# Optimization experiments

Measured on AMD Instinct MI355X. Metric: run time of the kernel, lower is better.

The kernel has to match this reference:

```python
import jax, jax.numpy as jnp
import numpy as np

L_KERNELS = 15
STRIDE = 1
DIMS = [60, 72, 86, 86, 71, 59]  # indim=4*15, then *1.2,*1.2, mid, /1.2,/1.2 per __init__


def setup_inputs() -> dict:
    key = jax.random.key(0)
    ks = jax.random.split(key, 13)
    B, C, L, K = 16, 4, 1000, 64
    inp = {"x": jax.random.normal(ks[0], (B, C, L), jnp.float32)}
    for i in range(5):
        di, do = DIMS[i], DIMS[i + 1]
        inp[f"w{i}"] = jax.random.normal(ks[1 + 2 * i], (K, di, do), jnp.float32) * (1.0 / np.sqrt(di))
        inp[f"b{i}"] = jax.random.normal(ks[2 + 2 * i], (K, do), jnp.float32) * 0.01
    inp["head_w"] = jax.random.normal(ks[11], (DIMS[5], 1), jnp.float32) * (1.0 / np.sqrt(DIMS[5]))
    inp["head_b"] = jax.random.normal(ks[12], (1,), jnp.float32) * 0.01
    return inp


def reference(x, w0, b0, w1, b1, w2, b2, w3, b3, w4, b4, head_w, head_b):
    B, C, L = x.shape
    l, s = L_KERNELS, STRIDE
    n_out = (L - l) // s + 1
    # unfold: (B, C, n_out, l) via gather of sliding windows
    idx = jnp.arange(n_out)[:, None] * s + jnp.arange(l)[None, :]
    xw = x[:, :, idx]
    # transpose(-2,-3) then flatten(start_dim=3): (B, n_out, C*l)
    xw = jnp.transpose(xw, (0, 2, 1, 3)).reshape(B, n_out, C * l)
    # per-kernel FC stack: broadcast-mul+sum in torch == grouped matmul here
    h = jax.nn.gelu(jnp.einsum('bld,kde->bkle', xw, w0) + b0[None, :, None, :], approximate=False)
    for w, b in ((w1, b1), (w2, b2), (w3, b3), (w4, b4)):
        h = jax.nn.gelu(jnp.einsum('bkld,kde->bkle', h, w) + b[None, :, None, :], approximate=False)
    out = (h @ head_w + head_b).squeeze(-1)  # (B, K, n_out)
    return out
```

## Files before the change

### kernel.cpp

```cpp
#include <hip/hip_runtime.h>

typedef _Float16 f16;
typedef __attribute__((ext_vector_type(8))) _Float16 f16x8;
typedef __attribute__((ext_vector_type(2))) __fp16 hf16x2;
typedef __attribute__((ext_vector_type(4))) float f32x4;

constexpr int C_ = 4, L_ = 1000, K_ = 64, NOUT = 986, NPOS = 16 * 986;
constexpr int TPB  = 256;
constexpr int MTB  = 128;
constexpr int NBLK = (NPOS + MTB - 1) / MTB;
constexpr int AST  = 104;
constexpr int ACT_EL  = MTB * AST;
constexpr size_t SMEM_BYTES = (size_t)ACT_EL * 2 + 480 * 4 + 64 * 4;

constexpr size_t WOFF[5]  = {0, 638976, 1277952, 1916928, 2555904};
constexpr int    WROWS[5] = {80, 96, 96, 80, 64};
constexpr int    DIv[5]   = {60, 72, 86, 86, 71};
constexpr int    DOv[5]   = {72, 86, 86, 71, 59};
constexpr size_t WTOT    = WOFF[4] + (size_t)K_ * 96 * AST;
constexpr size_t ACT_WS  = WTOT;
constexpr size_t WS_NEED = (WTOT + (size_t)NBLK * ACT_EL) * 2;

constexpr int WUNITS = 5 * K_ * 2;
constexpr int AUNITS = NBLK * 2;

__device__ __forceinline__ float gelu_f(float x) {
    float x2 = x * x;
    float ei = x * __builtin_fmaf(-0.1029433270f, x2, -2.3022082020f);
    float e  = __builtin_amdgcn_exp2f(ei);
    return x * __builtin_amdgcn_rcpf(e + 1.0f);
}

template<int MT>
__device__ __forceinline__ void pre_a(const f16* __restrict__ wsrc, f16x8 (&ap)[6],
                                      int li, int q) {
#pragma unroll
    for (int mt = 0; mt < MT; mt++)
        ap[mt] = *(const f16x8*)(wsrc + (mt * 16 + li) * AST + q * 8);
}

template<int KSTEPS, int MT>
__device__ __forceinline__ void layer_mm_p(const f16* __restrict__ actw,
                                           const f16* __restrict__ wsrc,
                                           const f16x8 (&ap)[6],
                                           f32x4 (&acc)[MT][2],
                                           const float* __restrict__ bl, int li, int q) {
#pragma unroll
    for (int mt = 0; mt < MT; mt++) {
        f32x4 bb = *(const f32x4*)(bl + mt * 16 + q * 4);
#pragma unroll
        for (int nt = 0; nt < 2; nt++) acc[mt][nt] = bb;
    }
#pragma unroll
    for (int ks = 0; ks < KSTEPS; ks++) {
        const int koff = ks * 32 + q * 8;
        f16x8 a[MT], b[2];
#pragma unroll
        for (int mt = 0; mt < MT; mt++)
            a[mt] = (ks == 0) ? ap[mt]
                              : *(const f16x8*)(wsrc + (mt * 16 + li) * AST + koff);
#pragma unroll
        for (int nt = 0; nt < 2; nt++)
            b[nt] = *(const f16x8*)(actw + (nt * 16 + li) * AST + koff);
#pragma unroll
        for (int mt = 0; mt < MT; mt++)
#pragma unroll
            for (int nt = 0; nt < 2; nt++)
                acc[mt][nt] = __builtin_amdgcn_mfma_f32_16x16x32_f16(a[mt], b[nt], acc[mt][nt], 0, 0, 0);
    }
}

template<int MT>
__device__ __forceinline__ void epilogue(f32x4 (&acc)[MT][2], f16* __restrict__ actw,
                                         int li, int q) {
#pragma unroll
    for (int mt = 0; mt < MT; mt++) {
        const int eb = mt * 16 + q * 4;
#pragma unroll
        for (int nt = 0; nt < 2; nt++) {
            union { hf16x2 h[2]; unsigned long long u; } pk;
            pk.h[0] = __builtin_amdgcn_cvt_pkrtz(gelu_f(acc[mt][nt][0]),
                                                 gelu_f(acc[mt][nt][1]));
            pk.h[1] = __builtin_amdgcn_cvt_pkrtz(gelu_f(acc[mt][nt][2]),
                                                 gelu_f(acc[mt][nt][3]));
            f16* dst = actw + (nt * 16 + li) * AST + eb;
            *(unsigned long long*)dst = pk.u;
        }
    }
}

template<int L>
__device__ __forceinline__ void prep_one_half(const float* __restrict__ wsrc0,
                                              f16* __restrict__ ws, f16* __restrict__ wl,
                                              int k, int h, int tid) {
    constexpr int DI = DIv[L], DO = DOv[L], RW = WROWS[L];
    const float* wsrc = wsrc0 + (size_t)k * DI * DO;
    constexpr int TOT = DI * DO;
    constexpr int NIT = (TOT + 255) / 256;
    float v[NIT];
#pragma unroll
    for (int it = 0; it < NIT; it++) {
        int i = tid + it * 256;
        v[it] = (i < TOT) ? wsrc[i] : 0.f;
    }
#pragma unroll
    for (int it = 0; it < NIT; it++) {
        int i = tid + it * 256;
        if (i < TOT) {
            int d = i / DO, e = i - d * DO;
            wl[d * 87 + e] = (f16)v[it];
        }
    }
    __syncthreads();
    f16* dst = ws + WOFF[L] + (size_t)k * 96 * AST;
    constexpr int HCH = (RW / 2) * 13;
    constexpr int NIT2 = (HCH + 255) / 256;
#pragma unroll
    for (int it = 0; it < NIT2; it++) {
        int c0 = tid + it * 256;
        if (c0 < HCH) {
            int c = h * HCH + c0;
            int e = c / 13, db = (c - e * 13) * 8;
            f16x8 vv;
#pragma unroll
            for (int j = 0; j < 8; j++) {
                int d = db + j;
                vv[j] = (e < DO && d < DI) ? wl[d * 87 + e] : (f16)0.f;
            }
            *(f16x8*)(dst + (size_t)c * 8) = vv;
        }
    }
}

__device__ __forceinline__ void prep_act_half(const float* __restrict__ x,
                                              f16* __restrict__ dst0, int m, int h, int tid) {
    if (m >= NBLK) return;
    f16* dst = dst0 + (size_t)m * ACT_EL;
    const int base = m * MTB;
    constexpr int HCHK = MTB * 13 / 2;
    for (int i0 = tid; i0 < HCHK; i0 += 256) {
        int i = h * HCHK + i0;
        int r = i / 13, cc = (i - r * 13) * 8;
        int p = base + r; if (p > NPOS - 1) p = NPOS - 1;
        int b = p / NOUT, pos = p - b * NOUT;
        f16x8 vv;
#pragma unroll
        for (int j = 0; j < 8; j++) {
            int c = cc + j;
            float v = 0.f;
            if (c < 60) { int ch = c / 15, jj = c - ch * 15; v = x[(size_t)(b * C_ + ch) * L_ + pos + jj]; }
            vv[j] = (f16)v;
        }
        *(f16x8*)(dst + (size_t)r * AST + cc) = vv;
    }
}

__global__ __launch_bounds__(256) void prep_all(
    const float* __restrict__ w0, const float* __restrict__ w1, const float* __restrict__ w2,
    const float* __restrict__ w3, const float* __restrict__ w4,
    const float* __restrict__ x, f16* __restrict__ ws) {
    __shared__ f16 wl[86 * 87];
    const int tid = threadIdx.x, u = blockIdx.x;
    if (u < WUNITS) {
        const int k = (u >> 1) & 63, h = u & 1;
        switch (u >> 7) {
            case 0: prep_one_half<0>(w0, ws, wl, k, h, tid); break;
            case 1: prep_one_half<1>(w1, ws, wl, k, h, tid); break;
            case 2: prep_one_half<2>(w2, ws, wl, k, h, tid); break;
            case 3: prep_one_half<3>(w3, ws, wl, k, h, tid); break;
            default: prep_one_half<4>(w4, ws, wl, k, h, tid); break;
        }
    } else {
        const int v = u - WUNITS;
        prep_act_half(x, ws + ACT_WS, v >> 1, v & 1, tid);
    }
}

template<bool PRE>
__global__ __launch_bounds__(TPB, 5) void mlp_main(
    const float* __restrict__ x,
    const float* __restrict__ b0, const float* __restrict__ b1, const float* __restrict__ b2,
    const float* __restrict__ b3, const float* __restrict__ b4,
    const float* __restrict__ hw, const float* __restrict__ hb,
    const f16* __restrict__ ws, float* __restrict__ out) {
    extern __shared__ char smemraw[];
    f16*   act   = (f16*)smemraw;
    float* biasl = (float*)(act + ACT_EL);
    float* headl = biasl + 480;

    const int tid = threadIdx.x, k = blockIdx.x, mblk = blockIdx.y;
    const int wv = tid >> 6, lane = tid & 63, li = lane & 15, q = lane >> 4;
    const int base = mblk * MTB;
    f16* actw = act + (wv * 32) * AST;
    const f16* wk = ws + (size_t)k * 96 * AST;

    f16x8 ap[6];
    pre_a<5>(wk + WOFF[0], ap, li, q);

    for (int i = tid; i < 480; i += TPB) {
        int l = i / 96, e = i - l * 96;
        const float* bg = (l == 0) ? b0 : (l == 1) ? b1 : (l == 2) ? b2 : (l == 3) ? b3 : b4;
        int DO = (l == 0) ? 72 : (l == 1) ? 86 : (l == 2) ? 86 : (l == 3) ? 71 : 59;
        biasl[i] = (e < DO) ? bg[k * DO + e] : 0.f;
    }
    if (tid < 64) headl[tid] = (tid < 59) ? hw[tid] : 0.f;

    if constexpr (PRE) {
        const f16* src = ws + ACT_WS + (size_t)mblk * ACT_EL;
        for (int c = wv; c < 26; c += 4) {
            __builtin_amdgcn_global_load_lds(
                (const __attribute__((address_space(1))) void*)(src + c * 512 + lane * 8),
                (__attribute__((address_space(3))) void*)(act + c * 512), 16, 0, 0);
        }
    } else {
        const int b0i = base / NOUT;
        const int thr = (b0i + 1) * NOUT;
        for (int i = tid; i < 64 * MTB; i += TPB) {
            int d = i >> 7, r = i & (MTB - 1);
            int p = base + r; if (p > NPOS - 1) p = NPOS - 1;
            int b = (p >= thr) ? b0i + 1 : b0i;
            int pos = p - b * NOUT;
            float v = 0.f;
            if (d < 60) { int c = d / 15, j = d - c * 15; v = x[(size_t)(b * C_ + c) * L_ + pos + j]; }
            act[r * AST + d] = (f16)v;
        }
        for (int i = tid; i < MTB * 2; i += TPB) {
            int r = i >> 1, cc = (i & 1) << 3;
            *(f16x8*)(act + r * AST + 80 + cc) = f16x8{0,0,0,0,0,0,0,0};
        }
    }
    const float hb0 = hb[0];
    __syncthreads();

    f32x4 acc[6][2];
    f32x4 (&acc5)[5][2] = reinterpret_cast<f32x4 (&)[5][2]>(acc);

    layer_mm_p<2, 5>(actw, wk + WOFF[0], ap, acc5, biasl + 0 * 96, li, q);
    pre_a<6>(wk + WOFF[1], ap, li, q);
    epilogue<5>(acc5, actw, li, q);
    layer_mm_p<3, 6>(actw, wk + WOFF[1], ap, acc, biasl + 1 * 96, li, q);
    pre_a<6>(wk + WOFF[2], ap, li, q);
    epilogue<6>(acc, actw, li, q);
    layer_mm_p<3, 6>(actw, wk + WOFF[2], ap, acc, biasl + 2 * 96, li, q);
    pre_a<5>(wk + WOFF[3], ap, li, q);
    epilogue<6>(acc, actw, li, q);
    layer_mm_p<3, 5>(actw, wk + WOFF[3], ap, acc5, biasl + 3 * 96, li, q);
    pre_a<4>(wk + WOFF[4], ap, li, q);
    epilogue<5>(acc5, actw, li, q);

    f32x4 acc4[4][2];
    layer_mm_p<3, 4>(actw, wk + WOFF[4], ap, acc4, biasl + 4 * 96, li, q);
    float sum[2] = {0.f, 0.f};
#pragma unroll
    for (int mt = 0; mt < 4; mt++) {
        const int eb = mt * 16 + q * 4;
        f32x4 hh = *(const f32x4*)(headl + eb);
#pragma unroll
        for (int nt = 0; nt < 2; nt++) {
#pragma unroll
            for (int r = 0; r < 4; r++)
                sum[nt] += gelu_f(acc4[mt][nt][r]) * hh[r];
        }
    }
#pragma unroll
    for (int nt = 0; nt < 2; nt++) {
        float s = sum[nt];
        s += __shfl_xor(s, 16);
        s += __shfl_xor(s, 32);
        s += hb0;
        if (lane < 16) {
            int p = base + wv * 32 + nt * 16 + lane;
            if (p < NPOS) {
                int b = p / NOUT, pos = p - b * NOUT;
                out[((size_t)(b * K_ + k)) * NOUT + pos] = s;
            }
        }
    }
}

extern "C" void kernel_launch(void* const* d_in, const int* in_sizes, int n_in,
                              void* d_out, int out_size, void* d_ws, size_t ws_size,
                              hipStream_t stream) {
    const float* x  = (const float*)d_in[0];
    const float* w0 = (const float*)d_in[1];  const float* b0 = (const float*)d_in[2];
    const float* w1 = (const float*)d_in[3];  const float* b1 = (const float*)d_in[4];
    const float* w2 = (const float*)d_in[5];  const float* b2 = (const float*)d_in[6];
    const float* w3 = (const float*)d_in[7];  const float* b3 = (const float*)d_in[8];
    const float* w4 = (const float*)d_in[9];  const float* b4 = (const float*)d_in[10];
    const float* hw = (const float*)d_in[11]; const float* hb = (const float*)d_in[12];
    float* out = (float*)d_out;
    f16* ws = (f16*)d_ws;

    const bool pre = (ws_size >= WS_NEED);

    if (pre) {
        (void)hipFuncSetAttribute((const void*)mlp_main<true>,
                                  hipFuncAttributeMaxDynamicSharedMemorySize, (int)SMEM_BYTES);
        prep_all<<<dim3(WUNITS + AUNITS), 256, 0, stream>>>(w0, w1, w2, w3, w4, x, ws);
        mlp_main<true><<<dim3(K_, NBLK), TPB, SMEM_BYTES, stream>>>(
            x, b0, b1, b2, b3, b4, hw, hb, ws, out);
    } else {
        (void)hipFuncSetAttribute((const void*)mlp_main<false>,
                                  hipFuncAttributeMaxDynamicSharedMemorySize, (int)SMEM_BYTES);
        prep_all<<<dim3(WUNITS), 256, 0, stream>>>(w0, w1, w2, w3, w4, x, ws);
        mlp_main<false><<<dim3(K_, NBLK), TPB, SMEM_BYTES, stream>>>(
            x, b0, b1, b2, b3, b4, hw, hb, ws, out);
    }
}
```

Measured before the change: 253.6 us.

## Halve position tile to 64 rows per block and drop weight-fragment prefetch

Cuts the position tile per block from 128 to 64, so each wave handles 16 positions with one B fragment instead of two. It also drops the cross-layer prefetch of the first weight k-step and raises the launch-bounds occupancy hint from 5 to 8. The smaller tile lowers LDS and register use to fit more resident blocks and doubles the grid, at the cost of half the weight reuse per LDS-loaded A fragment. The loss of the prefetch exposes weight-load latency at the start of each layer.

```diff
diff --git a/kernel.cpp b/kernel.cpp
--- a/kernel.cpp
+++ b/kernel.cpp
@@ -7,7 +7,7 @@
 
 constexpr int C_ = 4, L_ = 1000, K_ = 64, NOUT = 986, NPOS = 16 * 986;
 constexpr int TPB  = 256;
-constexpr int MTB  = 128;
+constexpr int MTB  = 64;
 constexpr int NBLK = (NPOS + MTB - 1) / MTB;
 constexpr int AST  = 104;
 constexpr int ACT_EL  = MTB * AST;
@@ -22,7 +22,7 @@
 constexpr size_t WS_NEED = (WTOT + (size_t)NBLK * ACT_EL) * 2;
 
 constexpr int WUNITS = 5 * K_ * 2;
-constexpr int AUNITS = NBLK * 2;
+constexpr int AUNITS = NBLK;
 
 __device__ __forceinline__ float gelu_f(float x) {
     float x2 = x * x;
@@ -31,61 +31,38 @@
     return x * __builtin_amdgcn_rcpf(e + 1.0f);
 }
 
-template<int MT>
-__device__ __forceinline__ void pre_a(const f16* __restrict__ wsrc, f16x8 (&ap)[6],
-                                      int li, int q) {
+template<int KSTEPS, int MT>
+__device__ __forceinline__ void layer_mm(const f16* __restrict__ actw,
+                                         const f16* __restrict__ wsrc,
+                                         f32x4 (&acc)[MT],
+                                         const float* __restrict__ bl, int li, int q) {
 #pragma unroll
     for (int mt = 0; mt < MT; mt++)
-        ap[mt] = *(const f16x8*)(wsrc + (mt * 16 + li) * AST + q * 8);
-}
-
-template<int KSTEPS, int MT>
-__device__ __forceinline__ void layer_mm_p(const f16* __restrict__ actw,
-                                           const f16* __restrict__ wsrc,
-                                           const f16x8 (&ap)[6],
-                                           f32x4 (&acc)[MT][2],
-                                           const float* __restrict__ bl, int li, int q) {
-#pragma unroll
-    for (int mt = 0; mt < MT; mt++) {
-        f32x4 bb = *(const f32x4*)(bl + mt * 16 + q * 4);
-#pragma unroll
-        for (int nt = 0; nt < 2; nt++) acc[mt][nt] = bb;
-    }
+        acc[mt] = *(const f32x4*)(bl + mt * 16 + q * 4);
 #pragma unroll
     for (int ks = 0; ks < KSTEPS; ks++) {
         const int koff = ks * 32 + q * 8;
-        f16x8 a[MT], b[2];
+        f16x8 a[MT];
 #pragma unroll
         for (int mt = 0; mt < MT; mt++)
-            a[mt] = (ks == 0) ? ap[mt]
-                              : *(const f16x8*)(wsrc + (mt * 16 + li) * AST + koff);
-#pragma unroll
-        for (int nt = 0; nt < 2; nt++)
-            b[nt] = *(const f16x8*)(actw + (nt * 16 + li) * AST + koff);
+            a[mt] = *(const f16x8*)(wsrc + (mt * 16 + li) * AST + koff);
+        f16x8 b = *(const f16x8*)(actw + li * AST + koff);
 #pragma unroll
         for (int mt = 0; mt < MT; mt++)
-#pragma unroll
-            for (int nt = 0; nt < 2; nt++)
-                acc[mt][nt] = __builtin_amdgcn_mfma_f32_16x16x32_f16(a[mt], b[nt], acc[mt][nt], 0, 0, 0);
+            acc[mt] = __builtin_amdgcn_mfma_f32_16x16x32_f16(a[mt], b, acc[mt], 0, 0, 0);
     }
 }
 
 template<int MT>
-__device__ __forceinline__ void epilogue(f32x4 (&acc)[MT][2], f16* __restrict__ actw,
+__device__ __forceinline__ void epilogue(f32x4 (&acc)[MT], f16* __restrict__ actw,
                                          int li, int q) {
 #pragma unroll
     for (int mt = 0; mt < MT; mt++) {
         const int eb = mt * 16 + q * 4;
-#pragma unroll
-        for (int nt = 0; nt < 2; nt++) {
-            union { hf16x2 h[2]; unsigned long long u; } pk;
-            pk.h[0] = __builtin_amdgcn_cvt_pkrtz(gelu_f(acc[mt][nt][0]),
-                                                 gelu_f(acc[mt][nt][1]));
-            pk.h[1] = __builtin_amdgcn_cvt_pkrtz(gelu_f(acc[mt][nt][2]),
-                                                 gelu_f(acc[mt][nt][3]));
-            f16* dst = actw + (nt * 16 + li) * AST + eb;
-            *(unsigned long long*)dst = pk.u;
-        }
+        union { hf16x2 h[2]; unsigned long long u; } pk;
+        pk.h[0] = __builtin_amdgcn_cvt_pkrtz(gelu_f(acc[mt][0]), gelu_f(acc[mt][1]));
+        pk.h[1] = __builtin_amdgcn_cvt_pkrtz(gelu_f(acc[mt][2]), gelu_f(acc[mt][3]));
+        *(unsigned long long*)(actw + li * AST + eb) = pk.u;
     }
 }
 
@@ -132,14 +109,13 @@
     }
 }
 
-__device__ __forceinline__ void prep_act_half(const float* __restrict__ x,
-                                              f16* __restrict__ dst0, int m, int h, int tid) {
+__device__ __forceinline__ void prep_act(const float* __restrict__ x, f16* __restrict__ dst0,
+                                         int m, int tid) {
     if (m >= NBLK) return;
     f16* dst = dst0 + (size_t)m * ACT_EL;
     const int base = m * MTB;
-    constexpr int HCHK = MTB * 13 / 2;
-    for (int i0 = tid; i0 < HCHK; i0 += 256) {
-        int i = h * HCHK + i0;
+    constexpr int CHK = MTB * 13;
+    for (int i = tid; i < CHK; i += 256) {
         int r = i / 13, cc = (i - r * 13) * 8;
         int p = base + r; if (p > NPOS - 1) p = NPOS - 1;
         int b = p / NOUT, pos = p - b * NOUT;
@@ -171,13 +147,12 @@
             default: prep_one_half<4>(w4, ws, wl, k, h, tid); break;
         }
     } else {
-        const int v = u - WUNITS;
-        prep_act_half(x, ws + ACT_WS, v >> 1, v & 1, tid);
+        prep_act(x, ws + ACT_WS, u - WUNITS, tid);
     }
 }
 
 template<bool PRE>
-__global__ __launch_bounds__(TPB, 5) void mlp_main(
+__global__ __launch_bounds__(TPB, 8) void mlp_main(
     const float* __restrict__ x,
     const float* __restrict__ b0, const float* __restrict__ b1, const float* __restrict__ b2,
     const float* __restrict__ b3, const float* __restrict__ b4,
@@ -191,11 +166,8 @@
     const int tid = threadIdx.x, k = blockIdx.x, mblk = blockIdx.y;
     const int wv = tid >> 6, lane = tid & 63, li = lane & 15, q = lane >> 4;
     const int base = mblk * MTB;
-    f16* actw = act + (wv * 32) * AST;
+    f16* actw = act + (wv * 16) * AST;
     const f16* wk = ws + (size_t)k * 96 * AST;
-
-    f16x8 ap[6];
-    pre_a<5>(wk + WOFF[0], ap, li, q);
 
     for (int i = tid; i < 480; i += TPB) {
         int l = i / 96, e = i - l * 96;
@@ -207,7 +179,7 @@
 
     if constexpr (PRE) {
         const f16* src = ws + ACT_WS + (size_t)mblk * ACT_EL;
-        for (int c = wv; c < 26; c += 4) {
+        for (int c = wv; c < 13; c += 4) {
             __builtin_amdgcn_global_load_lds(
                 (const __attribute__((address_space(1))) void*)(src + c * 512 + lane * 8),
                 (__attribute__((address_space(3))) void*)(act + c * 512), 16, 0, 0);
@@ -216,7 +188,7 @@
         const int b0i = base / NOUT;
         const int thr = (b0i + 1) * NOUT;
         for (int i = tid; i < 64 * MTB; i += TPB) {
-            int d = i >> 7, r = i & (MTB - 1);
+            int d = i >> 6, r = i & (MTB - 1);
             int p = base + r; if (p > NPOS - 1) p = NPOS - 1;
             int b = (p >= thr) ? b0i + 1 : b0i;
             int pos = p - b * NOUT;
@@ -232,48 +204,37 @@
     const float hb0 = hb[0];
     __syncthreads();
 
-    f32x4 acc[6][2];
-    f32x4 (&acc5)[5][2] = reinterpret_cast<f32x4 (&)[5][2]>(acc);
-
-    layer_mm_p<2, 5>(actw, wk + WOFF[0], ap, acc5, biasl + 0 * 96, li, q);
-    pre_a<6>(wk + WOFF[1], ap, li, q);
+    f32x4 acc[6];
+    f32x4 (&acc5)[5] = reinterpret_cast<f32x4 (&)[5]>(acc);
+
+    layer_mm<2, 5>(actw, wk + WOFF[0], acc5, biasl + 0 * 96, li, q);
     epilogue<5>(acc5, actw, li, q);
-    layer_mm_p<3, 6>(actw, wk + WOFF[1], ap, acc, biasl + 1 * 96, li, q);
-    pre_a<6>(wk + WOFF[2], ap, li, q);
+    layer_mm<3, 6>(actw, wk + WOFF[1], acc,  biasl + 1 * 96, li, q);
     epilogue<6>(acc, actw, li, q);
-    layer_mm_p<3, 6>(actw, wk + WOFF[2], ap, acc, biasl + 2 * 96, li, q);
-    pre_a<5>(wk + WOFF[3], ap, li, q);
+    layer_mm<3, 6>(actw, wk + WOFF[2], acc,  biasl + 2 * 96, li, q);
     epilogue<6>(acc, actw, li, q);
-    layer_mm_p<3, 5>(actw, wk + WOFF[3], ap, acc5, biasl + 3 * 96, li, q);
-    pre_a<4>(wk + WOFF[4], ap, li, q);
+    layer_mm<3, 5>(actw, wk + WOFF[3], acc5, biasl + 3 * 96, li, q);
     epilogue<5>(acc5, actw, li, q);
 
-    f32x4 acc4[4][2];
-    layer_mm_p<3, 4>(actw, wk + WOFF[4], ap, acc4, biasl + 4 * 96, li, q);
-    float sum[2] = {0.f, 0.f};
+    f32x4 acc4[4];
+    layer_mm<3, 4>(actw, wk + WOFF[4], acc4, biasl + 4 * 96, li, q);
+    float sum = 0.f;
 #pragma unroll
     for (int mt = 0; mt < 4; mt++) {
         const int eb = mt * 16 + q * 4;
         f32x4 hh = *(const f32x4*)(headl + eb);
 #pragma unroll
-        for (int nt = 0; nt < 2; nt++) {
-#pragma unroll
-            for (int r = 0; r < 4; r++)
-                sum[nt] += gelu_f(acc4[mt][nt][r]) * hh[r];
-        }
-    }
-#pragma unroll
-    for (int nt = 0; nt < 2; nt++) {
-        float s = sum[nt];
-        s += __shfl_xor(s, 16);
-        s += __shfl_xor(s, 32);
-        s += hb0;
-        if (lane < 16) {
-            int p = base + wv * 32 + nt * 16 + lane;
-            if (p < NPOS) {
-                int b = p / NOUT, pos = p - b * NOUT;
-                out[((size_t)(b * K_ + k)) * NOUT + pos] = s;
-            }
+        for (int r = 0; r < 4; r++)
+            sum += gelu_f(acc4[mt][r]) * hh[r];
+    }
+    sum += __shfl_xor(sum, 16);
+    sum += __shfl_xor(sum, 32);
+    sum += hb0;
+    if (lane < 16) {
+        int p = base + wv * 16 + lane;
+        if (p < NPOS) {
+            int b = p / NOUT, pos = p - b * NOUT;
+            out[((size_t)(b * K_ + k)) * NOUT + pos] = sum;
         }
     }
 }
```

After: 358.1 us. 41.2% more time.

## Stage per-layer weight panels into LDS via async global-to-LDS loads

Applied to the files above, without the earlier changes.

Each layer's per-kernel weight panel now goes into a shared LDS buffer with global_load_lds, and the MFMA A-operands are read from LDS instead of each wave reading them directly from global memory. All four waves share one panel copy, which cuts duplicate global traffic. The cost is extra LDS per block, with launch bounds lowered from 5 to 3 blocks per CU, and block-wide barriers between layers, which reduce overlap and occupancy.

```diff
diff --git a/kernel.cpp b/kernel.cpp
--- a/kernel.cpp
+++ b/kernel.cpp
@@ -11,12 +11,14 @@
 constexpr int NBLK = (NPOS + MTB - 1) / MTB;
 constexpr int AST  = 104;
 constexpr int ACT_EL  = MTB * AST;
-constexpr size_t SMEM_BYTES = (size_t)ACT_EL * 2 + 480 * 4 + 64 * 4;
+constexpr int WPAN_EL = 20 * 512;
+constexpr size_t SMEM_BYTES = (size_t)ACT_EL * 2 + (size_t)WPAN_EL * 2 + 480 * 4 + 64 * 4;
 
 constexpr size_t WOFF[5]  = {0, 638976, 1277952, 1916928, 2555904};
 constexpr int    WROWS[5] = {80, 96, 96, 80, 64};
 constexpr int    DIv[5]   = {60, 72, 86, 86, 71};
 constexpr int    DOv[5]   = {72, 86, 86, 71, 59};
+constexpr int    NCH[5]   = {17, 20, 20, 17, 13};
 constexpr size_t WTOT    = WOFF[4] + (size_t)K_ * 96 * AST;
 constexpr size_t ACT_WS  = WTOT;
 constexpr size_t WS_NEED = (WTOT + (size_t)NBLK * ACT_EL) * 2;
@@ -31,18 +33,18 @@
     return x * __builtin_amdgcn_rcpf(e + 1.0f);
 }
 
-template<int MT>
-__device__ __forceinline__ void pre_a(const f16* __restrict__ wsrc, f16x8 (&ap)[6],
-                                      int li, int q) {
-#pragma unroll
-    for (int mt = 0; mt < MT; mt++)
-        ap[mt] = *(const f16x8*)(wsrc + (mt * 16 + li) * AST + q * 8);
+__device__ __forceinline__ void stage_panel(const f16* __restrict__ src, f16* wpan,
+                                            int nch, int wv, int lane) {
+    for (int c = wv; c < nch; c += 4) {
+        __builtin_amdgcn_global_load_lds(
+            (const __attribute__((address_space(1))) void*)(src + c * 512 + lane * 8),
+            (__attribute__((address_space(3))) void*)(wpan + c * 512), 16, 0, 0);
+    }
 }
 
 template<int KSTEPS, int MT>
-__device__ __forceinline__ void layer_mm_p(const f16* __restrict__ actw,
-                                           const f16* __restrict__ wsrc,
-                                           const f16x8 (&ap)[6],
+__device__ __forceinline__ void layer_mm_l(const f16* __restrict__ actw,
+                                           const f16* __restrict__ wpan,
                                            f32x4 (&acc)[MT][2],
                                            const float* __restrict__ bl, int li, int q) {
 #pragma unroll
@@ -57,8 +59,7 @@
         f16x8 a[MT], b[2];
 #pragma unroll
         for (int mt = 0; mt < MT; mt++)
-            a[mt] = (ks == 0) ? ap[mt]
-                              : *(const f16x8*)(wsrc + (mt * 16 + li) * AST + koff);
+            a[mt] = *(const f16x8*)(wpan + (mt * 16 + li) * AST + koff);
 #pragma unroll
         for (int nt = 0; nt < 2; nt++)
             b[nt] = *(const f16x8*)(actw + (nt * 16 + li) * AST + koff);
@@ -177,7 +178,7 @@
 }
 
 template<bool PRE>
-__global__ __launch_bounds__(TPB, 5) void mlp_main(
+__global__ __launch_bounds__(TPB, 3) void mlp_main(
     const float* __restrict__ x,
     const float* __restrict__ b0, const float* __restrict__ b1, const float* __restrict__ b2,
     const float* __restrict__ b3, const float* __restrict__ b4,
@@ -185,7 +186,8 @@
     const f16* __restrict__ ws, float* __restrict__ out) {
     extern __shared__ char smemraw[];
     f16*   act   = (f16*)smemraw;
-    float* biasl = (float*)(act + ACT_EL);
+    f16*   wpan  = act + ACT_EL;
+    float* biasl = (float*)(wpan + WPAN_EL);
     float* headl = biasl + 480;
 
     const int tid = threadIdx.x, k = blockIdx.x, mblk = blockIdx.y;
@@ -194,8 +196,7 @@
     f16* actw = act + (wv * 32) * AST;
     const f16* wk = ws + (size_t)k * 96 * AST;
 
-    f16x8 ap[6];
-    pre_a<5>(wk + WOFF[0], ap, li, q);
+    stage_panel(wk + WOFF[0], wpan, NCH[0], wv, lane);
 
     for (int i = tid; i < 480; i += TPB) {
         int l = i / 96, e = i - l * 96;
@@ -235,21 +236,32 @@
     f32x4 acc[6][2];
     f32x4 (&acc5)[5][2] = reinterpret_cast<f32x4 (&)[5][2]>(acc);
 
-    layer_mm_p<2, 5>(actw, wk + WOFF[0], ap, acc5, biasl + 0 * 96, li, q);
-    pre_a<6>(wk + WOFF[1], ap, li, q);
+    layer_mm_l<2, 5>(actw, wpan, acc5, biasl + 0 * 96, li, q);
+    __syncthreads();
+    stage_panel(wk + WOFF[1], wpan, NCH[1], wv, lane);
     epilogue<5>(acc5, actw, li, q);
-    layer_mm_p<3, 6>(actw, wk + WOFF[1], ap, acc, biasl + 1 * 96, li, q);
-    pre_a<6>(wk + WOFF[2], ap, li, q);
+    __syncthreads();
+
+    layer_mm_l<3, 6>(actw, wpan, acc, biasl + 1 * 96, li, q);
+    __syncthreads();
+    stage_panel(wk + WOFF[2], wpan, NCH[2], wv, lane);
     epilogue<6>(acc, actw, li, q);
-    layer_mm_p<3, 6>(actw, wk + WOFF[2], ap, acc, biasl + 2 * 96, li, q);
-    pre_a<5>(wk + WOFF[3], ap, li, q);
+    __syncthreads();
+
+    layer_mm_l<3, 6>(actw, wpan, acc, biasl + 2 * 96, li, q);
+    __syncthreads();
+    stage_panel(wk + WOFF[3], wpan, NCH[3], wv, lane);
     epilogue<6>(acc, actw, li, q);
-    layer_mm_p<3, 5>(actw, wk + WOFF[3], ap, acc5, biasl + 3 * 96, li, q);
-    pre_a<4>(wk + WOFF[4], ap, li, q);
+    __syncthreads();
+
+    layer_mm_l<3, 5>(actw, wpan, acc5, biasl + 3 * 96, li, q);
+    __syncthreads();
+    stage_panel(wk + WOFF[4], wpan, NCH[4], wv, lane);
     epilogue<5>(acc5, actw, li, q);
+    __syncthreads();
 
     f32x4 acc4[4][2];
-    layer_mm_p<3, 4>(actw, wk + WOFF[4], ap, acc4, biasl + 4 * 96, li, q);
+    layer_mm_l<3, 4>(actw, wpan, acc4, biasl + 4 * 96, li, q);
     float sum[2] = {0.f, 0.f};
 #pragma unroll
     for (int mt = 0; mt < 4; mt++) {
```

Result: no change. 248.8 us (-1.9%).
